# Kernel tuning notes

Measured on AMD Instinct MI355X. Metric: run time of the kernel, lower is better.

## Reference

```python
import jax, jax.numpy as jnp
import numpy as np

N_VARS = 64
HID = 256
BATCH = 16384


def setup_inputs() -> dict:
    key = jax.random.key(0)
    ks = jax.random.split(key, 9)
    X = jax.random.normal(ks[0], (BATCH, N_VARS), dtype=jnp.float32)
    U = jax.random.normal(ks[1], (BATCH, N_VARS), dtype=jnp.float32)
    # Strictly upper-triangular random binary adjacency -> guaranteed DAG,
    # identity order (0..n-1) is a valid topological order.
    rng = np.random.default_rng(0)
    G = np.triu(rng.integers(0, 2, size=(N_VARS, N_VARS)), k=1).astype(np.int32)
    causal_graph = jnp.asarray(G)
    # Per-variable 3-layer MLP params, stacked over the variable axis.
    # torch.nn.Linear default init: U(-1/sqrt(fan_in), 1/sqrt(fan_in)).
    s1 = 1.0 / np.sqrt(N_VARS + 1)
    s2 = 1.0 / np.sqrt(HID)
    s3 = 1.0 / np.sqrt(HID // 2)
    W1 = jax.random.uniform(ks[2], (N_VARS, N_VARS + 1, HID), jnp.float32, -s1, s1)
    b1 = jax.random.uniform(ks[3], (N_VARS, HID), jnp.float32, -s1, s1)
    W2 = jax.random.uniform(ks[4], (N_VARS, HID, HID // 2), jnp.float32, -s2, s2)
    b2 = jax.random.uniform(ks[5], (N_VARS, HID // 2), jnp.float32, -s2, s2)
    W3 = jax.random.uniform(ks[6], (N_VARS, HID // 2, 1), jnp.float32, -s3, s3)
    b3 = jax.random.uniform(ks[7], (N_VARS, 1), jnp.float32, -s3, s3)
    return {"X": X, "U": U, "causal_graph": causal_graph,
            "W1": W1, "b1": b1, "W2": W2, "b2": b2, "W3": W3, "b3": b3}


def reference(X, U, causal_graph, W1, b1, W2, b2, W3, b3):
    n = causal_graph.shape[0]
    # mask[i, j] = 1 if j is a parent of i (graph[j, i] > 0)
    mask = (causal_graph > 0).T.astype(X.dtype)  # [n, n]
    Ut = U.T  # [n, B]

    def step(Y, xs):
        i, m, u, w1, c1, w2, c2, w3, c3 = xs
        x_in = Y * m                                    # zero non-parents, [B, n]
        inp = jnp.concatenate([x_in, u[:, None]], axis=-1)  # [B, n+1]
        h = jax.nn.relu(inp @ w1 + c1)                  # [B, HID]
        h = jax.nn.relu(h @ w2 + c2)                    # [B, HID//2]
        y = (h @ w3 + c3)[:, 0]                         # [B]
        Y = Y.at[:, i].set(y)
        return Y, None

    idx = jnp.arange(n)
    Y, _ = jax.lax.scan(step, X, (idx, mask, Ut, W1, b1, W2, b2, W3, b3))
    return Y
```

## Files before the change

### kernel.cpp

```cpp
#include <hip/hip_runtime.h>

#define BATCH 16384
#define RT    32

typedef unsigned short u16;
typedef __attribute__((ext_vector_type(8))) short short8;
typedef __attribute__((ext_vector_type(8))) _Float16 f16x8;
typedef __attribute__((ext_vector_type(4))) float f32x4;
typedef __attribute__((ext_vector_type(4))) unsigned int u32x4;

__device__ __forceinline__ u16 f2h(float x) {
    union { _Float16 h; u16 u; } c; c.h = (_Float16)x; return c.u;
}
__device__ __forceinline__ float h2f(u16 b) {
    union { u16 u; _Float16 h; } c; c.u = b; return (float)c.h;
}
__device__ __forceinline__ unsigned int pk2(float a, float b) {
    union { __attribute__((ext_vector_type(2))) __fp16 v; unsigned int u; } c;
    c.v = __builtin_amdgcn_cvt_pkrtz(a, b);
    return c.u;
}
__device__ __forceinline__ float red16(float x) {
    x += __builtin_bit_cast(float, __builtin_amdgcn_update_dpp(
             0, __builtin_bit_cast(int, x), 0xB1, 0xF, 0xF, true));
    x += __builtin_bit_cast(float, __builtin_amdgcn_update_dpp(
             0, __builtin_bit_cast(int, x), 0x4E, 0xF, 0xF, true));
    x += __builtin_bit_cast(float, __builtin_amdgcn_update_dpp(
             0, __builtin_bit_cast(int, x), 0x124, 0xF, 0xF, true));
    x += __builtin_bit_cast(float, __builtin_amdgcn_update_dpp(
             0, __builtin_bit_cast(int, x), 0x128, 0xF, 0xF, true));
    return x;
}

__global__ void prep_w1(const float* __restrict__ W1, const int* __restrict__ G,
                        u16* __restrict__ P) {
    int idx = blockIdx.x * 256 + threadIdx.x;
    int n = idx & 255;
    int k = (idx >> 8) & 63;
    int v = idx >> 14;
    float w = (k + 1 < v && G[k * 64 + v] > 0) ? W1[((size_t)v * 65 + k) * 256 + n] : 0.0f;
    P[(((size_t)(v * 8 + (k >> 3)) * 256 + n) << 3) + (k & 7)] = f2h(w);
}
__global__ void prep_we(const float* __restrict__ W1, const int* __restrict__ G,
                        u16* __restrict__ P) {
    int dim = threadIdx.x;
    int v   = blockIdx.x;
    float wu = W1[((size_t)v * 65 + 64) * 256 + dim];
    float wp = (v >= 1 && G[(v - 1) * 64 + v] > 0)
                   ? W1[((size_t)v * 65 + (v - 1)) * 256 + dim] : 0.0f;
    size_t o = ((size_t)v * 256 + dim) << 3;
    P[o + 0] = f2h(wu);
    P[o + 1] = f2h(wp);
    #pragma unroll
    for (int j = 2; j < 8; ++j) P[o + j] = 0;
}
__global__ void prep_w2(const float* __restrict__ W2, u16* __restrict__ P) {
    int idx = blockIdx.x * 256 + threadIdx.x;
    int n = idx & 127;
    int k = (idx >> 7) & 255;
    int v = idx >> 15;
    P[(((size_t)(v * 32 + (k >> 3)) * 128 + n) << 3) + (k & 7)] =
        f2h(W2[((size_t)v * 256 + k) * 128 + n]);
}

#define AST   72
#define H1ST  264
#define YOST  68
#define UST   68

__global__ __launch_bounds__(512, 4)
void sen_fused(const float* __restrict__ U,
               const u16* __restrict__ P1, const u16* __restrict__ P2,
               const u16* __restrict__ Pe,
               const float* __restrict__ b1, const float* __restrict__ b2,
               const float* __restrict__ W3, const float* __restrict__ b3,
               float* __restrict__ Y)
{
    __shared__ __attribute__((aligned(16))) u16 Ay[RT * AST];
    __shared__ __attribute__((aligned(16))) u16 h1[RT * H1ST];
    __shared__ __attribute__((aligned(16))) float yp[RT][12];
    __shared__ __attribute__((aligned(16))) float Yout[RT * YOST];
    __shared__ __attribute__((aligned(16))) float Ut[RT * UST];

    const int tid  = threadIdx.x;
    const int row0 = blockIdx.x * RT;

    {
        short8 z = {0,0,0,0,0,0,0,0};
        for (int i = tid; i < (RT * AST) / 8; i += 512)
            *(short8*)&Ay[i * 8] = z;
        if (tid < RT * 12) ((float*)yp)[tid] = 0.0f;
        const int row = tid >> 4, c4 = (tid & 15) * 4;
        *(f32x4*)&Ut[row * UST + c4] =
            *(const f32x4*)(U + (size_t)(row0 + row) * 64 + c4);
    }
    __syncthreads();

    const int w  = tid >> 6, l = tid & 63;
    const int lr = l & 15,  lk = l >> 4;
    const int mg = w;
    const int cg = w;

    int o_p1[2][2], o_p2[8], o_pe[2];
    #pragma unroll
    for (int kt = 0; kt < 2; ++kt)
        #pragma unroll
        for (int ni = 0; ni < 2; ++ni)
            o_p1[kt][ni] = (((kt * 4 + lk) * 256) + mg * 32 + ni * 16 + lr) << 3;
    #pragma unroll
    for (int kt = 0; kt < 8; ++kt)
        o_p2[kt] = (((kt * 4 + lk) * 128) + cg * 16 + lr) << 3;
    #pragma unroll
    for (int ni = 0; ni < 2; ++ni)
        o_pe[ni] = (mg * 32 + ni * 16 + lr) << 3;
    const int dimc  = mg * 32 + lk * 4;
    const int colc  = cg * 16 + lr;
    const int urow0 = lr * UST, urow1 = (16 + lr) * UST;

    f32x4 acc1[2][2];
    f16x8 we[2];
    float u_c[2], b2c, w3c, b3p;
    {
        #pragma unroll
        for (int ni = 0; ni < 2; ++ni) {
            const f32x4 b1v = *(const f32x4*)(b1 + dimc + ni * 16);
            acc1[0][ni] = b1v;
            acc1[1][ni] = b1v;
            we[ni] = *(const f16x8*)&Pe[o_pe[ni]];
        }
        u_c[0] = Ut[urow0];
        u_c[1] = Ut[urow1];
        b2c = b2[colc];
        w3c = W3[colc];
        b3p = 0.0f;
    }

    #pragma unroll 1
    for (int v = 0; v < 64; ++v) {
        const u16*   P1v = P1 + (size_t)(v + 1) * 16384;
        const u16*   P2v = P2 + (size_t)v * 32768;
        const u16*   Pev = Pe + (size_t)(v + 1) * 2048;
        const float* b1p = b1 + (v + 1) * 256;
        const float* b2p = b2 + (v + 1) * 128;
        const float* W3p = W3 + (v + 1) * 128;

        float yprev[2];
        #pragma unroll
        for (int nj = 0; nj < 2; ++nj) {
            const int row = nj * 16 + lr;
            const f32x4 a = *(const f32x4*)&yp[row][0];
            const f32x4 b = *(const f32x4*)&yp[row][4];
            yprev[nj] = b3p + a[0] + a[1] + a[2] + a[3] + b[0] + b[1] + b[2] + b[3];
        }
        if (v > 0 && w == 0 && lk == 0) {
            Ay[lr * AST + (v - 1)]        = f2h(yprev[0]);
            Ay[(16 + lr) * AST + (v - 1)] = f2h(yprev[1]);
            Yout[lr * YOST + (v - 1)]        = yprev[0];
            Yout[(16 + lr) * YOST + (v - 1)] = yprev[1];
        }
        #pragma unroll
        for (int nj = 0; nj < 2; ++nj) {
            const unsigned int pk_e = (lk == 0) ? pk2(u_c[nj], yprev[nj]) : 0u;
            const u32x4 t = {pk_e, 0u, 0u, 0u};
            const f16x8 Yfe = __builtin_bit_cast(f16x8, t);
            #pragma unroll
            for (int ni = 0; ni < 2; ++ni)
                acc1[nj][ni] = __builtin_amdgcn_mfma_f32_16x16x32_f16(we[ni], Yfe, acc1[nj][ni], 0, 0, 0);
        }
        #pragma unroll
        for (int nj = 0; nj < 2; ++nj) {
            const int brow = nj * 16 + lr;
            #pragma unroll
            for (int ni = 0; ni < 2; ++ni) {
                float x[4];
                #pragma unroll
                for (int r = 0; r < 4; ++r)
                    x[r] = fmaxf(acc1[nj][ni][r], 0.0f);
                unsigned long long pk = (unsigned long long)pk2(x[0], x[1])
                                      | ((unsigned long long)pk2(x[2], x[3]) << 32);
                *(unsigned long long*)&h1[brow * H1ST + mg * 32 + ni * 16 + lk * 4] = pk;
            }
        }
        __syncthreads();

        f32x4 acc2[2];
        acc2[0] = (f32x4){b2c, b2c, b2c, b2c};
        acc2[1] = acc2[0];
        #pragma unroll
        for (int kt = 0; kt < 8; ++kt) {
            const f16x8 Bf = *(const f16x8*)&P2v[o_p2[kt]];
            #pragma unroll
            for (int mi = 0; mi < 2; ++mi) {
                const f16x8 Hf = *(const f16x8*)&h1[(mi * 16 + lr) * H1ST + kt * 32 + lk * 8];
                acc2[mi] = __builtin_amdgcn_mfma_f32_16x16x32_f16(Hf, Bf, acc2[mi], 0, 0, 0);
            }
        }
        #pragma unroll
        for (int mi = 0; mi < 2; ++mi) {
            float s0 = red16(fmaxf(acc2[mi][0], 0.0f) * w3c);
            float s1 = red16(fmaxf(acc2[mi][1], 0.0f) * w3c);
            float s2 = red16(fmaxf(acc2[mi][2], 0.0f) * w3c);
            float s3 = red16(fmaxf(acc2[mi][3], 0.0f) * w3c);
            if (lr == 0) {
                const int row = mi * 16 + lk * 4;
                yp[row + 0][cg] = s0;
                yp[row + 1][cg] = s1;
                yp[row + 2][cg] = s2;
                yp[row + 3][cg] = s3;
            }
        }
        if (v < 63) {
            #pragma unroll
            for (int ni = 0; ni < 2; ++ni) {
                const f32x4 nb1 = *(const f32x4*)(b1p + dimc + ni * 16);
                acc1[0][ni] = nb1;
                acc1[1][ni] = nb1;
            }
            #pragma unroll
            for (int kt = 0; kt < 2; ++kt) {
                f16x8 Yf[2];
                #pragma unroll
                for (int nj = 0; nj < 2; ++nj)
                    Yf[nj] = *(const f16x8*)&Ay[(nj * 16 + lr) * AST + kt * 32 + lk * 8];
                #pragma unroll
                for (int ni = 0; ni < 2; ++ni) {
                    const f16x8 Wf = *(const f16x8*)&P1v[o_p1[kt][ni]];
                    #pragma unroll
                    for (int nj = 0; nj < 2; ++nj)
                        acc1[nj][ni] = __builtin_amdgcn_mfma_f32_16x16x32_f16(Wf, Yf[nj], acc1[nj][ni], 0, 0, 0);
                }
            }
            we[0] = *(const f16x8*)&Pev[o_pe[0]];
            we[1] = *(const f16x8*)&Pev[o_pe[1]];
            u_c[0] = Ut[urow0 + v + 1];
            u_c[1] = Ut[urow1 + v + 1];
            b2c = b2p[colc];
            w3c = W3p[colc];
            b3p = b3[v];
        }
        __syncthreads();
    }

    if (w == 0 && lk == 0) {
        #pragma unroll
        for (int nj = 0; nj < 2; ++nj) {
            const int row = nj * 16 + lr;
            const f32x4 a = *(const f32x4*)&yp[row][0];
            const f32x4 b = *(const f32x4*)&yp[row][4];
            Yout[row * YOST + 63] =
                b3[63] + a[0] + a[1] + a[2] + a[3] + b[0] + b[1] + b[2] + b[3];
        }
    }
    __syncthreads();
    {
        const int row = tid >> 4, c4 = (tid & 15) * 4;
        *(float4*)(Y + (size_t)(row0 + row) * 64 + c4) = *(float4*)&Yout[row * YOST + c4];
    }
}

extern "C" void kernel_launch(void* const* d_in, const int* in_sizes, int n_in,
                              void* d_out, int out_size, void* d_ws, size_t ws_size,
                              hipStream_t stream) {
    const float* U  = (const float*)d_in[1];
    const int*   G  = (const int*)  d_in[2];
    const float* W1 = (const float*)d_in[3];
    const float* b1 = (const float*)d_in[4];
    const float* W2 = (const float*)d_in[5];
    const float* b2 = (const float*)d_in[6];
    const float* W3 = (const float*)d_in[7];
    const float* b3 = (const float*)d_in[8];
    float* Y = (float*)d_out;

    const size_t S1 = (size_t)64 * 64 * 256;
    const size_t S2 = (size_t)64 * 256 * 128;
    u16* P1 = (u16*)d_ws;
    u16* P2 = P1 + S1;
    u16* Pe = P2 + S2;

    prep_w1<<<(64 * 64 * 256) / 256, 256, 0, stream>>>(W1, G, P1);
    prep_w2<<<(64 * 256 * 128) / 256, 256, 0, stream>>>(W2, P2);
    prep_we<<<64, 256, 0, stream>>>(W1, G, Pe);
    sen_fused<<<BATCH / RT, 512, 0, stream>>>(U, P1, P2, Pe, b1, b2, W3, b3, Y);
}
```

Measured before the change: 212.2 us.

## Split row halves across 16 waves per block instead of 8

Doubles the block to 1024 threads so each wave owns one 16-row half of the 32-row tile instead of both halves. This halves the MFMA chain and register footprint per wave and adds wave-level parallelism to the serial 64-step dependency chain. The cost is that weight fragments from global or L2 are now loaded twice per block (once per half), and each barrier synchronises twice as many waves.

```diff
diff --git a/kernel.cpp b/kernel.cpp
--- a/kernel.cpp
+++ b/kernel.cpp
@@ -68,7 +68,7 @@
 #define YOST  68
 #define UST   68
 
-__global__ __launch_bounds__(512, 4)
+__global__ __launch_bounds__(1024, 8)
 void sen_fused(const float* __restrict__ U,
                const u16* __restrict__ P1, const u16* __restrict__ P2,
                const u16* __restrict__ Pe,
@@ -87,19 +87,21 @@
 
     {
         short8 z = {0,0,0,0,0,0,0,0};
-        for (int i = tid; i < (RT * AST) / 8; i += 512)
+        for (int i = tid; i < (RT * AST) / 8; i += 1024)
             *(short8*)&Ay[i * 8] = z;
         if (tid < RT * 12) ((float*)yp)[tid] = 0.0f;
-        const int row = tid >> 4, c4 = (tid & 15) * 4;
-        *(f32x4*)&Ut[row * UST + c4] =
-            *(const f32x4*)(U + (size_t)(row0 + row) * 64 + c4);
+        if (tid < RT * 16) {
+            const int row = tid >> 4, c4 = (tid & 15) * 4;
+            *(f32x4*)&Ut[row * UST + c4] =
+                *(const f32x4*)(U + (size_t)(row0 + row) * 64 + c4);
+        }
     }
     __syncthreads();
 
     const int w  = tid >> 6, l = tid & 63;
     const int lr = l & 15,  lk = l >> 4;
-    const int mg = w;
-    const int cg = w;
+    const int mg = w & 7, nj = w >> 3;
+    const int cg = w & 7, mi = w >> 3;
 
     int o_p1[2][2], o_p2[8], o_pe[2];
     #pragma unroll
@@ -113,23 +115,24 @@
     #pragma unroll
     for (int ni = 0; ni < 2; ++ni)
         o_pe[ni] = (mg * 32 + ni * 16 + lr) << 3;
-    const int dimc  = mg * 32 + lk * 4;
-    const int colc  = cg * 16 + lr;
-    const int urow0 = lr * UST, urow1 = (16 + lr) * UST;
-
-    f32x4 acc1[2][2];
+    const int dimc   = mg * 32 + lk * 4;
+    const int colc   = cg * 16 + lr;
+    const int myrow  = nj * 16 + lr;
+    const int urow   = myrow * UST;
+    const int ayrow  = myrow * AST;
+    const int h1wb   = myrow * H1ST + mg * 32 + lk * 4;
+    const int h1rrow = (mi * 16 + lr) * H1ST;
+
+    f32x4 acc1[2];
     f16x8 we[2];
-    float u_c[2], b2c, w3c, b3p;
+    float u_c, b2c, w3c, b3p;
     {
         #pragma unroll
         for (int ni = 0; ni < 2; ++ni) {
-            const f32x4 b1v = *(const f32x4*)(b1 + dimc + ni * 16);
-            acc1[0][ni] = b1v;
-            acc1[1][ni] = b1v;
+            acc1[ni] = *(const f32x4*)(b1 + dimc + ni * 16);
             we[ni] = *(const f16x8*)&Pe[o_pe[ni]];
         }
-        u_c[0] = Ut[urow0];
-        u_c[1] = Ut[urow1];
+        u_c = Ut[urow];
         b2c = b2[colc];
         w3c = W3[colc];
         b3p = 0.0f;
@@ -144,63 +147,48 @@
         const float* b2p = b2 + (v + 1) * 128;
         const float* W3p = W3 + (v + 1) * 128;
 
-        float yprev[2];
-        #pragma unroll
-        for (int nj = 0; nj < 2; ++nj) {
-            const int row = nj * 16 + lr;
-            const f32x4 a = *(const f32x4*)&yp[row][0];
-            const f32x4 b = *(const f32x4*)&yp[row][4];
-            yprev[nj] = b3p + a[0] + a[1] + a[2] + a[3] + b[0] + b[1] + b[2] + b[3];
-        }
-        if (v > 0 && w == 0 && lk == 0) {
-            Ay[lr * AST + (v - 1)]        = f2h(yprev[0]);
-            Ay[(16 + lr) * AST + (v - 1)] = f2h(yprev[1]);
-            Yout[lr * YOST + (v - 1)]        = yprev[0];
-            Yout[(16 + lr) * YOST + (v - 1)] = yprev[1];
-        }
-        #pragma unroll
-        for (int nj = 0; nj < 2; ++nj) {
-            const unsigned int pk_e = (lk == 0) ? pk2(u_c[nj], yprev[nj]) : 0u;
+        float yprev;
+        {
+            const f32x4 a = *(const f32x4*)&yp[myrow][0];
+            const f32x4 b = *(const f32x4*)&yp[myrow][4];
+            yprev = b3p + a[0] + a[1] + a[2] + a[3] + b[0] + b[1] + b[2] + b[3];
+        }
+        if (v > 0 && (w == 0 || w == 8) && lk == 0) {
+            Ay[ayrow + (v - 1)] = f2h(yprev);
+            Yout[myrow * YOST + (v - 1)] = yprev;
+        }
+        {
+            const unsigned int pk_e = (lk == 0) ? pk2(u_c, yprev) : 0u;
             const u32x4 t = {pk_e, 0u, 0u, 0u};
             const f16x8 Yfe = __builtin_bit_cast(f16x8, t);
             #pragma unroll
             for (int ni = 0; ni < 2; ++ni)
-                acc1[nj][ni] = __builtin_amdgcn_mfma_f32_16x16x32_f16(we[ni], Yfe, acc1[nj][ni], 0, 0, 0);
-        }
-        #pragma unroll
-        for (int nj = 0; nj < 2; ++nj) {
-            const int brow = nj * 16 + lr;
-            #pragma unroll
-            for (int ni = 0; ni < 2; ++ni) {
-                float x[4];
-                #pragma unroll
-                for (int r = 0; r < 4; ++r)
-                    x[r] = fmaxf(acc1[nj][ni][r], 0.0f);
-                unsigned long long pk = (unsigned long long)pk2(x[0], x[1])
-                                      | ((unsigned long long)pk2(x[2], x[3]) << 32);
-                *(unsigned long long*)&h1[brow * H1ST + mg * 32 + ni * 16 + lk * 4] = pk;
-            }
+                acc1[ni] = __builtin_amdgcn_mfma_f32_16x16x32_f16(we[ni], Yfe, acc1[ni], 0, 0, 0);
+        }
+        #pragma unroll
+        for (int ni = 0; ni < 2; ++ni) {
+            float x[4];
+            #pragma unroll
+            for (int r = 0; r < 4; ++r)
+                x[r] = fmaxf(acc1[ni][r], 0.0f);
+            unsigned long long pk = (unsigned long long)pk2(x[0], x[1])
+                                  | ((unsigned long long)pk2(x[2], x[3]) << 32);
+            *(unsigned long long*)&h1[h1wb + ni * 16] = pk;
         }
         __syncthreads();
 
-        f32x4 acc2[2];
-        acc2[0] = (f32x4){b2c, b2c, b2c, b2c};
-        acc2[1] = acc2[0];
+        f32x4 acc2 = (f32x4){b2c, b2c, b2c, b2c};
         #pragma unroll
         for (int kt = 0; kt < 8; ++kt) {
             const f16x8 Bf = *(const f16x8*)&P2v[o_p2[kt]];
-            #pragma unroll
-            for (int mi = 0; mi < 2; ++mi) {
-                const f16x8 Hf = *(const f16x8*)&h1[(mi * 16 + lr) * H1ST + kt * 32 + lk * 8];
-                acc2[mi] = __builtin_amdgcn_mfma_f32_16x16x32_f16(Hf, Bf, acc2[mi], 0, 0, 0);
-            }
-        }
-        #pragma unroll
-        for (int mi = 0; mi < 2; ++mi) {
-            float s0 = red16(fmaxf(acc2[mi][0], 0.0f) * w3c);
-            float s1 = red16(fmaxf(acc2[mi][1], 0.0f) * w3c);
-            float s2 = red16(fmaxf(acc2[mi][2], 0.0f) * w3c);
-            float s3 = red16(fmaxf(acc2[mi][3], 0.0f) * w3c);
+            const f16x8 Hf = *(const f16x8*)&h1[h1rrow + kt * 32 + lk * 8];
+            acc2 = __builtin_amdgcn_mfma_f32_16x16x32_f16(Hf, Bf, acc2, 0, 0, 0);
+        }
+        {
+            float s0 = red16(fmaxf(acc2[0], 0.0f) * w3c);
+            float s1 = red16(fmaxf(acc2[1], 0.0f) * w3c);
+            float s2 = red16(fmaxf(acc2[2], 0.0f) * w3c);
+            float s3 = red16(fmaxf(acc2[3], 0.0f) * w3c);
             if (lr == 0) {
                 const int row = mi * 16 + lk * 4;
                 yp[row + 0][cg] = s0;
@@ -211,29 +199,20 @@
         }
         if (v < 63) {
             #pragma unroll
-            for (int ni = 0; ni < 2; ++ni) {
-                const f32x4 nb1 = *(const f32x4*)(b1p + dimc + ni * 16);
-                acc1[0][ni] = nb1;
-                acc1[1][ni] = nb1;
-            }
+            for (int ni = 0; ni < 2; ++ni)
+                acc1[ni] = *(const f32x4*)(b1p + dimc + ni * 16);
             #pragma unroll
             for (int kt = 0; kt < 2; ++kt) {
-                f16x8 Yf[2];
-                #pragma unroll
-                for (int nj = 0; nj < 2; ++nj)
-                    Yf[nj] = *(const f16x8*)&Ay[(nj * 16 + lr) * AST + kt * 32 + lk * 8];
+                const f16x8 Yf = *(const f16x8*)&Ay[ayrow + kt * 32 + lk * 8];
                 #pragma unroll
                 for (int ni = 0; ni < 2; ++ni) {
                     const f16x8 Wf = *(const f16x8*)&P1v[o_p1[kt][ni]];
-                    #pragma unroll
-                    for (int nj = 0; nj < 2; ++nj)
-                        acc1[nj][ni] = __builtin_amdgcn_mfma_f32_16x16x32_f16(Wf, Yf[nj], acc1[nj][ni], 0, 0, 0);
+                    acc1[ni] = __builtin_amdgcn_mfma_f32_16x16x32_f16(Wf, Yf, acc1[ni], 0, 0, 0);
                 }
             }
             we[0] = *(const f16x8*)&Pev[o_pe[0]];
             we[1] = *(const f16x8*)&Pev[o_pe[1]];
-            u_c[0] = Ut[urow0 + v + 1];
-            u_c[1] = Ut[urow1 + v + 1];
+            u_c = Ut[urow + v + 1];
             b2c = b2p[colc];
             w3c = W3p[colc];
             b3p = b3[v];
@@ -241,18 +220,14 @@
         __syncthreads();
     }
 
-    if (w == 0 && lk == 0) {
-        #pragma unroll
-        for (int nj = 0; nj < 2; ++nj) {
-            const int row = nj * 16 + lr;
-            const f32x4 a = *(const f32x4*)&yp[row][0];
-            const f32x4 b = *(const f32x4*)&yp[row][4];
-            Yout[row * YOST + 63] =
-                b3[63] + a[0] + a[1] + a[2] + a[3] + b[0] + b[1] + b[2] + b[3];
-        }
+    if ((w == 0 || w == 8) && lk == 0) {
+        const f32x4 a = *(const f32x4*)&yp[myrow][0];
+        const f32x4 b = *(const f32x4*)&yp[myrow][4];
+        Yout[myrow * YOST + 63] =
+            b3[63] + a[0] + a[1] + a[2] + a[3] + b[0] + b[1] + b[2] + b[3];
     }
     __syncthreads();
-    {
+    if (tid < RT * 16) {
         const int row = tid >> 4, c4 = (tid & 15) * 4;
         *(float4*)(Y + (size_t)(row0 + row) * 64 + c4) = *(float4*)&Yout[row * YOST + c4];
     }
@@ -280,5 +255,5 @@
     prep_w1<<<(64 * 64 * 256) / 256, 256, 0, stream>>>(W1, G, P1);
     prep_w2<<<(64 * 256 * 128) / 256, 256, 0, stream>>>(W2, P2);
     prep_we<<<64, 256, 0, stream>>>(W1, G, Pe);
-    sen_fused<<<BATCH / RT, 512, 0, stream>>>(U, P1, P2, Pe, b1, b2, W3, b3, Y);
-}
+    sen_fused<<<BATCH / RT, 1024, 0, stream>>>(U, P1, P2, Pe, b1, b2, W3, b3, Y);
+}
```

Result: slower. 300.9 us (+41.8%).

## Retile second-layer GEMM so each wave covers 16 rows by 32 columns

Applied to the files above, without the earlier changes.

The layer-2 work split changes from each wave owning 16 output columns across all 32 rows to each wave owning 16 rows by 32 columns. Each h1 fragment now feeds two MFMAs, and the partial-sum reduction needs only four column groups, which shrinks the yp buffer and the final sum. The W2 fragments for the whole step are also loaded into registers at the top of each iteration, so the global loads can overlap the layer-1 epilogue and the barrier. This holds more registers live, which could hurt occupancy at launch bounds of 512 threads and 4 blocks.

```diff
diff --git a/kernel.cpp b/kernel.cpp
--- a/kernel.cpp
+++ b/kernel.cpp
@@ -78,7 +78,7 @@
 {
     __shared__ __attribute__((aligned(16))) u16 Ay[RT * AST];
     __shared__ __attribute__((aligned(16))) u16 h1[RT * H1ST];
-    __shared__ __attribute__((aligned(16))) float yp[RT][12];
+    __shared__ __attribute__((aligned(16))) float yp[RT][8];
     __shared__ __attribute__((aligned(16))) float Yout[RT * YOST];
     __shared__ __attribute__((aligned(16))) float Ut[RT * UST];
 
@@ -89,7 +89,7 @@
         short8 z = {0,0,0,0,0,0,0,0};
         for (int i = tid; i < (RT * AST) / 8; i += 512)
             *(short8*)&Ay[i * 8] = z;
-        if (tid < RT * 12) ((float*)yp)[tid] = 0.0f;
+        if (tid < RT * 8) ((float*)yp)[tid] = 0.0f;
         const int row = tid >> 4, c4 = (tid & 15) * 4;
         *(f32x4*)&Ut[row * UST + c4] =
             *(const f32x4*)(U + (size_t)(row0 + row) * 64 + c4);
@@ -99,9 +99,9 @@
     const int w  = tid >> 6, l = tid & 63;
     const int lr = l & 15,  lk = l >> 4;
     const int mg = w;
-    const int cg = w;
-
-    int o_p1[2][2], o_p2[8], o_pe[2];
+    const int cg = w & 3, rh = w >> 2;
+
+    int o_p1[2][2], o_p2[8][2], o_pe[2];
     #pragma unroll
     for (int kt = 0; kt < 2; ++kt)
         #pragma unroll
@@ -109,17 +109,21 @@
             o_p1[kt][ni] = (((kt * 4 + lk) * 256) + mg * 32 + ni * 16 + lr) << 3;
     #pragma unroll
     for (int kt = 0; kt < 8; ++kt)
-        o_p2[kt] = (((kt * 4 + lk) * 128) + cg * 16 + lr) << 3;
+        #pragma unroll
+        for (int f = 0; f < 2; ++f)
+            o_p2[kt][f] = (((kt * 4 + lk) * 128) + cg * 32 + f * 16 + lr) << 3;
     #pragma unroll
     for (int ni = 0; ni < 2; ++ni)
         o_pe[ni] = (mg * 32 + ni * 16 + lr) << 3;
     const int dimc  = mg * 32 + lk * 4;
-    const int colc  = cg * 16 + lr;
+    const int colc0 = cg * 32 + lr;
+    const int colc1 = cg * 32 + 16 + lr;
     const int urow0 = lr * UST, urow1 = (16 + lr) * UST;
+    const int h1r   = (rh * 16 + lr) * H1ST;
 
     f32x4 acc1[2][2];
     f16x8 we[2];
-    float u_c[2], b2c, w3c, b3p;
+    float u_c[2], b2c[2], w3c[2], b3p;
     {
         #pragma unroll
         for (int ni = 0; ni < 2; ++ni) {
@@ -130,8 +134,8 @@
         }
         u_c[0] = Ut[urow0];
         u_c[1] = Ut[urow1];
-        b2c = b2[colc];
-        w3c = W3[colc];
+        b2c[0] = b2[colc0]; b2c[1] = b2[colc1];
+        w3c[0] = W3[colc0]; w3c[1] = W3[colc1];
         b3p = 0.0f;
     }
 
@@ -144,13 +148,19 @@
         const float* b2p = b2 + (v + 1) * 128;
         const float* W3p = W3 + (v + 1) * 128;
 
+        f16x8 p2f[8][2];
+        #pragma unroll
+        for (int kt = 0; kt < 8; ++kt) {
+            p2f[kt][0] = *(const f16x8*)&P2v[o_p2[kt][0]];
+            p2f[kt][1] = *(const f16x8*)&P2v[o_p2[kt][1]];
+        }
+
         float yprev[2];
         #pragma unroll
         for (int nj = 0; nj < 2; ++nj) {
             const int row = nj * 16 + lr;
             const f32x4 a = *(const f32x4*)&yp[row][0];
-            const f32x4 b = *(const f32x4*)&yp[row][4];
-            yprev[nj] = b3p + a[0] + a[1] + a[2] + a[3] + b[0] + b[1] + b[2] + b[3];
+            yprev[nj] = b3p + a[0] + a[1] + a[2] + a[3];
         }
         if (v > 0 && w == 0 && lk == 0) {
             Ay[lr * AST + (v - 1)]        = f2h(yprev[0]);
@@ -184,30 +194,21 @@
         __syncthreads();
 
         f32x4 acc2[2];
-        acc2[0] = (f32x4){b2c, b2c, b2c, b2c};
-        acc2[1] = acc2[0];
+        acc2[0] = (f32x4){b2c[0], b2c[0], b2c[0], b2c[0]};
+        acc2[1] = (f32x4){b2c[1], b2c[1], b2c[1], b2c[1]};
         #pragma unroll
         for (int kt = 0; kt < 8; ++kt) {
-            const f16x8 Bf = *(const f16x8*)&P2v[o_p2[kt]];
-            #pragma unroll
-            for (int mi = 0; mi < 2; ++mi) {
-                const f16x8 Hf = *(const f16x8*)&h1[(mi * 16 + lr) * H1ST + kt * 32 + lk * 8];
-                acc2[mi] = __builtin_amdgcn_mfma_f32_16x16x32_f16(Hf, Bf, acc2[mi], 0, 0, 0);
-            }
-        }
-        #pragma unroll
-        for (int mi = 0; mi < 2; ++mi) {
-            float s0 = red16(fmaxf(acc2[mi][0], 0.0f) * w3c);
-            float s1 = red16(fmaxf(acc2[mi][1], 0.0f) * w3c);
-            float s2 = red16(fmaxf(acc2[mi][2], 0.0f) * w3c);
-            float s3 = red16(fmaxf(acc2[mi][3], 0.0f) * w3c);
-            if (lr == 0) {
-                const int row = mi * 16 + lk * 4;
-                yp[row + 0][cg] = s0;
-                yp[row + 1][cg] = s1;
-                yp[row + 2][cg] = s2;
-                yp[row + 3][cg] = s3;
-            }
+            const f16x8 Hf = *(const f16x8*)&h1[h1r + kt * 32 + lk * 8];
+            acc2[0] = __builtin_amdgcn_mfma_f32_16x16x32_f16(Hf, p2f[kt][0], acc2[0], 0, 0, 0);
+            acc2[1] = __builtin_amdgcn_mfma_f32_16x16x32_f16(Hf, p2f[kt][1], acc2[1], 0, 0, 0);
+        }
+        #pragma unroll
+        for (int r = 0; r < 4; ++r) {
+            const float t = fmaxf(acc2[0][r], 0.0f) * w3c[0]
+                          + fmaxf(acc2[1][r], 0.0f) * w3c[1];
+            const float s = red16(t);
+            if (lr == 0)
+                yp[rh * 16 + lk * 4 + r][cg] = s;
         }
         if (v < 63) {
             #pragma unroll
@@ -234,8 +235,8 @@
             we[1] = *(const f16x8*)&Pev[o_pe[1]];
             u_c[0] = Ut[urow0 + v + 1];
             u_c[1] = Ut[urow1 + v + 1];
-            b2c = b2p[colc];
-            w3c = W3p[colc];
+            b2c[0] = b2p[colc0]; b2c[1] = b2p[colc1];
+            w3c[0] = W3p[colc0]; w3c[1] = W3p[colc1];
             b3p = b3[v];
         }
         __syncthreads();
@@ -246,9 +247,7 @@
         for (int nj = 0; nj < 2; ++nj) {
             const int row = nj * 16 + lr;
             const f32x4 a = *(const f32x4*)&yp[row][0];
-            const f32x4 b = *(const f32x4*)&yp[row][4];
-            Yout[row * YOST + 63] =
-                b3[63] + a[0] + a[1] + a[2] + a[3] + b[0] + b[1] + b[2] + b[3];
+            Yout[row * YOST + 63] = b3[63] + a[0] + a[1] + a[2] + a[3];
         }
     }
     __syncthreads();
```

After: 318.9 us. +50.3%, slower.

## Process two row tiles per block to reuse weight fragments across tiles

Applied to the files above, without the earlier changes.

Each block now handles two 32-row batch tiles at once, so every W1/W2 fragment loaded from global memory feeds twice as many MFMAs. Grid size is halved and launch bounds drop from 4 to 2 blocks per CU to make room for the doubled accumulators and shared buffers. The goal is to cut weight traffic and per-variable sync overhead per row. In exchange, register pressure and LDS use per block rise, and there are fewer blocks to hide latency.

```diff
diff --git a/kernel.cpp b/kernel.cpp
--- a/kernel.cpp
+++ b/kernel.cpp
@@ -68,7 +68,7 @@
 #define YOST  68
 #define UST   68
 
-__global__ __launch_bounds__(512, 4)
+__global__ __launch_bounds__(512, 2)
 void sen_fused(const float* __restrict__ U,
                const u16* __restrict__ P1, const u16* __restrict__ P2,
                const u16* __restrict__ Pe,
@@ -76,23 +76,26 @@
                const float* __restrict__ W3, const float* __restrict__ b3,
                float* __restrict__ Y)
 {
-    __shared__ __attribute__((aligned(16))) u16 Ay[RT * AST];
-    __shared__ __attribute__((aligned(16))) u16 h1[RT * H1ST];
-    __shared__ __attribute__((aligned(16))) float yp[RT][12];
-    __shared__ __attribute__((aligned(16))) float Yout[RT * YOST];
-    __shared__ __attribute__((aligned(16))) float Ut[RT * UST];
+    __shared__ __attribute__((aligned(16))) u16 Ay[2][RT * AST];
+    __shared__ __attribute__((aligned(16))) u16 h1[2][RT * H1ST];
+    __shared__ __attribute__((aligned(16))) float yp[2][RT][12];
+    __shared__ __attribute__((aligned(16))) float Yout[2][RT * YOST];
+    __shared__ __attribute__((aligned(16))) float Ut[2][RT * UST];
 
     const int tid  = threadIdx.x;
-    const int row0 = blockIdx.x * RT;
+    const int brow0 = blockIdx.x * (2 * RT);
 
     {
         short8 z = {0,0,0,0,0,0,0,0};
-        for (int i = tid; i < (RT * AST) / 8; i += 512)
-            *(short8*)&Ay[i * 8] = z;
-        if (tid < RT * 12) ((float*)yp)[tid] = 0.0f;
-        const int row = tid >> 4, c4 = (tid & 15) * 4;
-        *(f32x4*)&Ut[row * UST + c4] =
-            *(const f32x4*)(U + (size_t)(row0 + row) * 64 + c4);
+        #pragma unroll
+        for (int t = 0; t < 2; ++t) {
+            for (int i = tid; i < (RT * AST) / 8; i += 512)
+                *(short8*)&Ay[t][i * 8] = z;
+            if (tid < RT * 12) ((float*)yp[t])[tid] = 0.0f;
+            const int row = tid >> 4, c4 = (tid & 15) * 4;
+            *(f32x4*)&Ut[t][row * UST + c4] =
+                *(const f32x4*)(U + (size_t)(brow0 + t * RT + row) * 64 + c4);
+        }
     }
     __syncthreads();
 
@@ -117,19 +120,25 @@
     const int colc  = cg * 16 + lr;
     const int urow0 = lr * UST, urow1 = (16 + lr) * UST;
 
-    f32x4 acc1[2][2];
+    f32x4 acc1[2][2][2];
     f16x8 we[2];
-    float u_c[2], b2c, w3c, b3p;
+    float u_c[2][2], b2c, w3c, b3p;
     {
         #pragma unroll
         for (int ni = 0; ni < 2; ++ni) {
             const f32x4 b1v = *(const f32x4*)(b1 + dimc + ni * 16);
-            acc1[0][ni] = b1v;
-            acc1[1][ni] = b1v;
+            #pragma unroll
+            for (int t = 0; t < 2; ++t) {
+                acc1[t][0][ni] = b1v;
+                acc1[t][1][ni] = b1v;
+            }
             we[ni] = *(const f16x8*)&Pe[o_pe[ni]];
         }
-        u_c[0] = Ut[urow0];
-        u_c[1] = Ut[urow1];
+        #pragma unroll
+        for (int t = 0; t < 2; ++t) {
+            u_c[t][0] = Ut[t][urow0];
+            u_c[t][1] = Ut[t][urow1];
+        }
         b2c = b2[colc];
         w3c = W3[colc];
         b3p = 0.0f;
@@ -144,96 +153,123 @@
         const float* b2p = b2 + (v + 1) * 128;
         const float* W3p = W3 + (v + 1) * 128;
 
-        float yprev[2];
-        #pragma unroll
-        for (int nj = 0; nj < 2; ++nj) {
-            const int row = nj * 16 + lr;
-            const f32x4 a = *(const f32x4*)&yp[row][0];
-            const f32x4 b = *(const f32x4*)&yp[row][4];
-            yprev[nj] = b3p + a[0] + a[1] + a[2] + a[3] + b[0] + b[1] + b[2] + b[3];
-        }
+        float yprev[2][2];
+        #pragma unroll
+        for (int t = 0; t < 2; ++t)
+            #pragma unroll
+            for (int nj = 0; nj < 2; ++nj) {
+                const int row = nj * 16 + lr;
+                const f32x4 a = *(const f32x4*)&yp[t][row][0];
+                const f32x4 b = *(const f32x4*)&yp[t][row][4];
+                yprev[t][nj] = b3p + a[0] + a[1] + a[2] + a[3]
+                                   + b[0] + b[1] + b[2] + b[3];
+            }
         if (v > 0 && w == 0 && lk == 0) {
-            Ay[lr * AST + (v - 1)]        = f2h(yprev[0]);
-            Ay[(16 + lr) * AST + (v - 1)] = f2h(yprev[1]);
-            Yout[lr * YOST + (v - 1)]        = yprev[0];
-            Yout[(16 + lr) * YOST + (v - 1)] = yprev[1];
-        }
-        #pragma unroll
-        for (int nj = 0; nj < 2; ++nj) {
-            const unsigned int pk_e = (lk == 0) ? pk2(u_c[nj], yprev[nj]) : 0u;
-            const u32x4 t = {pk_e, 0u, 0u, 0u};
-            const f16x8 Yfe = __builtin_bit_cast(f16x8, t);
-            #pragma unroll
-            for (int ni = 0; ni < 2; ++ni)
-                acc1[nj][ni] = __builtin_amdgcn_mfma_f32_16x16x32_f16(we[ni], Yfe, acc1[nj][ni], 0, 0, 0);
-        }
-        #pragma unroll
-        for (int nj = 0; nj < 2; ++nj) {
-            const int brow = nj * 16 + lr;
-            #pragma unroll
-            for (int ni = 0; ni < 2; ++ni) {
-                float x[4];
-                #pragma unroll
-                for (int r = 0; r < 4; ++r)
-                    x[r] = fmaxf(acc1[nj][ni][r], 0.0f);
-                unsigned long long pk = (unsigned long long)pk2(x[0], x[1])
-                                      | ((unsigned long long)pk2(x[2], x[3]) << 32);
-                *(unsigned long long*)&h1[brow * H1ST + mg * 32 + ni * 16 + lk * 4] = pk;
-            }
-        }
+            #pragma unroll
+            for (int t = 0; t < 2; ++t) {
+                Ay[t][lr * AST + (v - 1)]        = f2h(yprev[t][0]);
+                Ay[t][(16 + lr) * AST + (v - 1)] = f2h(yprev[t][1]);
+                Yout[t][lr * YOST + (v - 1)]        = yprev[t][0];
+                Yout[t][(16 + lr) * YOST + (v - 1)] = yprev[t][1];
+            }
+        }
+        #pragma unroll
+        for (int t = 0; t < 2; ++t)
+            #pragma unroll
+            for (int nj = 0; nj < 2; ++nj) {
+                const unsigned int pk_e = (lk == 0) ? pk2(u_c[t][nj], yprev[t][nj]) : 0u;
+                const u32x4 tt = {pk_e, 0u, 0u, 0u};
+                const f16x8 Yfe = __builtin_bit_cast(f16x8, tt);
+                #pragma unroll
+                for (int ni = 0; ni < 2; ++ni)
+                    acc1[t][nj][ni] = __builtin_amdgcn_mfma_f32_16x16x32_f16(we[ni], Yfe, acc1[t][nj][ni], 0, 0, 0);
+            }
+        #pragma unroll
+        for (int t = 0; t < 2; ++t)
+            #pragma unroll
+            for (int nj = 0; nj < 2; ++nj) {
+                const int brow = nj * 16 + lr;
+                #pragma unroll
+                for (int ni = 0; ni < 2; ++ni) {
+                    float x[4];
+                    #pragma unroll
+                    for (int r = 0; r < 4; ++r)
+                        x[r] = fmaxf(acc1[t][nj][ni][r], 0.0f);
+                    unsigned long long pk = (unsigned long long)pk2(x[0], x[1])
+                                          | ((unsigned long long)pk2(x[2], x[3]) << 32);
+                    *(unsigned long long*)&h1[t][brow * H1ST + mg * 32 + ni * 16 + lk * 4] = pk;
+                }
+            }
         __syncthreads();
 
-        f32x4 acc2[2];
-        acc2[0] = (f32x4){b2c, b2c, b2c, b2c};
-        acc2[1] = acc2[0];
+        f32x4 acc2[2][2];
+        #pragma unroll
+        for (int t = 0; t < 2; ++t) {
+            acc2[t][0] = (f32x4){b2c, b2c, b2c, b2c};
+            acc2[t][1] = acc2[t][0];
+        }
         #pragma unroll
         for (int kt = 0; kt < 8; ++kt) {
             const f16x8 Bf = *(const f16x8*)&P2v[o_p2[kt]];
             #pragma unroll
+            for (int t = 0; t < 2; ++t)
+                #pragma unroll
+                for (int mi = 0; mi < 2; ++mi) {
+                    const f16x8 Hf = *(const f16x8*)&h1[t][(mi * 16 + lr) * H1ST + kt * 32 + lk * 8];
+                    acc2[t][mi] = __builtin_amdgcn_mfma_f32_16x16x32_f16(Hf, Bf, acc2[t][mi], 0, 0, 0);
+                }
+        }
+        #pragma unroll
+        for (int t = 0; t < 2; ++t)
+            #pragma unroll
             for (int mi = 0; mi < 2; ++mi) {
-                const f16x8 Hf = *(const f16x8*)&h1[(mi * 16 + lr) * H1ST + kt * 32 + lk * 8];
-                acc2[mi] = __builtin_amdgcn_mfma_f32_16x16x32_f16(Hf, Bf, acc2[mi], 0, 0, 0);
-            }
-        }
-        #pragma unroll
-        for (int mi = 0; mi < 2; ++mi) {
-            float s0 = red16(fmaxf(acc2[mi][0], 0.0f) * w3c);
-            float s1 = red16(fmaxf(acc2[mi][1], 0.0f) * w3c);
-            float s2 = red16(fmaxf(acc2[mi][2], 0.0f) * w3c);
-            float s3 = red16(fmaxf(acc2[mi][3], 0.0f) * w3c);
-            if (lr == 0) {
-                const int row = mi * 16 + lk * 4;
-                yp[row + 0][cg] = s0;
-                yp[row + 1][cg] = s1;
-                yp[row + 2][cg] = s2;
-                yp[row + 3][cg] = s3;
-            }
-        }
+                float s0 = red16(fmaxf(acc2[t][mi][0], 0.0f) * w3c);
+                float s1 = red16(fmaxf(acc2[t][mi][1], 0.0f) * w3c);
+                float s2 = red16(fmaxf(acc2[t][mi][2], 0.0f) * w3c);
+                float s3 = red16(fmaxf(acc2[t][mi][3], 0.0f) * w3c);
+                if (lr == 0) {
+                    const int row = mi * 16 + lk * 4;
+                    yp[t][row + 0][cg] = s0;
+                    yp[t][row + 1][cg] = s1;
+                    yp[t][row + 2][cg] = s2;
+                    yp[t][row + 3][cg] = s3;
+                }
+            }
         if (v < 63) {
             #pragma unroll
             for (int ni = 0; ni < 2; ++ni) {
                 const f32x4 nb1 = *(const f32x4*)(b1p + dimc + ni * 16);
-                acc1[0][ni] = nb1;
-                acc1[1][ni] = nb1;
+                #pragma unroll
+                for (int t = 0; t < 2; ++t) {
+                    acc1[t][0][ni] = nb1;
+                    acc1[t][1][ni] = nb1;
+                }
             }
             #pragma unroll
             for (int kt = 0; kt < 2; ++kt) {
-                f16x8 Yf[2];
-                #pragma unroll
-                for (int nj = 0; nj < 2; ++nj)
-                    Yf[nj] = *(const f16x8*)&Ay[(nj * 16 + lr) * AST + kt * 32 + lk * 8];
+                f16x8 Yf[2][2];
+                #pragma unroll
+                for (int t = 0; t < 2; ++t)
+                    #pragma unroll
+                    for (int nj = 0; nj < 2; ++nj)
+                        Yf[t][nj] = *(const f16x8*)&Ay[t][(nj * 16 + lr) * AST + kt * 32 + lk * 8];
                 #pragma unroll
                 for (int ni = 0; ni < 2; ++ni) {
                     const f16x8 Wf = *(const f16x8*)&P1v[o_p1[kt][ni]];
                     #pragma unroll
-                    for (int nj = 0; nj < 2; ++nj)
-                        acc1[nj][ni] = __builtin_amdgcn_mfma_f32_16x16x32_f16(Wf, Yf[nj], acc1[nj][ni], 0, 0, 0);
+                    for (int t = 0; t < 2; ++t)
+                        #pragma unroll
+                        for (int nj = 0; nj < 2; ++nj)
+                            acc1[t][nj][ni] = __builtin_amdgcn_mfma_f32_16x16x32_f16(Wf, Yf[t][nj], acc1[t][nj][ni], 0, 0, 0);
                 }
             }
             we[0] = *(const f16x8*)&Pev[o_pe[0]];
             we[1] = *(const f16x8*)&Pev[o_pe[1]];
-            u_c[0] = Ut[urow0 + v + 1];
-            u_c[1] = Ut[urow1 + v + 1];
+            #pragma unroll
+            for (int t = 0; t < 2; ++t) {
+                u_c[t][0] = Ut[t][urow0 + v + 1];
+                u_c[t][1] = Ut[t][urow1 + v + 1];
+            }
             b2c = b2p[colc];
             w3c = W3p[colc];
             b3p = b3[v];
@@ -243,18 +279,23 @@
 
     if (w == 0 && lk == 0) {
         #pragma unroll
-        for (int nj = 0; nj < 2; ++nj) {
-            const int row = nj * 16 + lr;
-            const f32x4 a = *(const f32x4*)&yp[row][0];
-            const f32x4 b = *(const f32x4*)&yp[row][4];
-            Yout[row * YOST + 63] =
-                b3[63] + a[0] + a[1] + a[2] + a[3] + b[0] + b[1] + b[2] + b[3];
-        }
+        for (int t = 0; t < 2; ++t)
+            #pragma unroll
+            for (int nj = 0; nj < 2; ++nj) {
+                const int row = nj * 16 + lr;
+                const f32x4 a = *(const f32x4*)&yp[t][row][0];
+                const f32x4 b = *(const f32x4*)&yp[t][row][4];
+                Yout[t][row * YOST + 63] =
+                    b3[63] + a[0] + a[1] + a[2] + a[3] + b[0] + b[1] + b[2] + b[3];
+            }
     }
     __syncthreads();
     {
         const int row = tid >> 4, c4 = (tid & 15) * 4;
-        *(float4*)(Y + (size_t)(row0 + row) * 64 + c4) = *(float4*)&Yout[row * YOST + c4];
+        #pragma unroll
+        for (int t = 0; t < 2; ++t)
+            *(float4*)(Y + (size_t)(brow0 + t * RT + row) * 64 + c4) =
+                *(float4*)&Yout[t][row * YOST + c4];
     }
 }
 
@@ -280,5 +321,5 @@
     prep_w1<<<(64 * 64 * 256) / 256, 256, 0, stream>>>(W1, G, P1);
     prep_w2<<<(64 * 256 * 128) / 256, 256, 0, stream>>>(W2, P2);
     prep_we<<<64, 256, 0, stream>>>(W1, G, Pe);
-    sen_fused<<<BATCH / RT, 512, 0, stream>>>(U, P1, P2, Pe, b1, b2, W3, b3, Y);
-}
+    sen_fused<<<BATCH / (2 * RT), 512, 0, stream>>>(U, P1, P2, Pe, b1, b2, W3, b3, Y);
+}
```

New measurement: 263.5 us. 24.2% more time.
